# Performance work log

Measured on AMD Instinct MI355X. Metric: run time of the kernel, lower is better.

## Reference

```python
import jax, jax.numpy as jnp
import numpy as np

# YOLOv4 finest head: layer_no = 2 -> stride 8, anchor mask [0,1,2]
ANCHORS = np.array([[12,16],[19,36],[40,28],[36,75],[76,55],[72,146],[142,110],[192,243],[459,401]], dtype=np.float32)
STRIDE = 8.0
ANCH_MASK = (0, 1, 2)
N_CLASSES = 80
IGNORE_THRESH = 0.7


def setup_inputs() -> dict:
    key = jax.random.key(0)
    k1, k2, k3, k4, k5, k6, k7 = jax.random.split(key, 7)
    B, A, F = 32, 3, 76
    n_ch = 5 + N_CLASSES
    N = 50  # max padded boxes per image
    # 'output' feeds BCELoss -> must be probabilities in (0,1)
    output = jnp.clip(jax.random.uniform(k1, (B, A, F, F, n_ch)), 1e-4, 1.0 - 1e-4)
    # decoded pred boxes in grid units: xy in [0,F), wh > 0
    pxy = jax.random.uniform(k2, (B, A, F, F, 2)) * F
    pwh = jax.random.uniform(k3, (B, A, F, F, 2)) * 7.5 + 0.5
    pred = jnp.concatenate([pxy, pwh], axis=-1)
    # padded labels [cls, x, y, w, h] in pixels; first n rows valid, rest zero
    cls = jax.random.randint(k4, (B, N, 1), 0, N_CLASSES).astype(jnp.float32)
    xy = jax.random.uniform(k5, (B, N, 2)) * 604.0 + 2.0
    wh = jax.random.uniform(k6, (B, N, 2)) * 112.0 + 8.0
    labels = jnp.concatenate([cls, xy, wh], axis=-1)
    nvalid = jax.random.randint(k7, (B, 1), 5, N + 1)
    labels = labels * (jnp.arange(N)[None, :] < nvalid)[..., None].astype(jnp.float32)
    return {"output": output, "pred": pred, "labels": labels}


def _safe_log(x):
    # torch BCELoss clamps log terms at -100
    return jnp.maximum(jnp.log(jnp.maximum(x, 1e-43)), -100.0)


def _bce_sum(p, t, w):
    return -jnp.sum(w * (t * _safe_log(p) + (1.0 - t) * _safe_log(1.0 - p)))


def _yolo_layer_loss(output, pred, labels):
    B, A, F = output.shape[0], output.shape[1], output.shape[2]
    n_ch = output.shape[-1]
    N = labels.shape[1]
    dt = output.dtype
    ag = jnp.asarray(ANCHORS, dtype=dt) / STRIDE            # [9,2] anchors in grid units
    ma = ag[jnp.asarray(ANCH_MASK)]                          # [3,2] masked anchors

    valid = (labels.sum(-1) > 0)                             # [B,N] real (non-pad) boxes
    vf = valid.astype(dt)
    tx = labels[..., 1] / STRIDE
    ty = labels[..., 2] / STRIDE
    tw = labels[..., 3] / STRIDE
    th = labels[..., 4] / STRIDE
    ti = tx.astype(jnp.int32)
    tj = ty.astype(jnp.int32)
    twm, thm = tw * vf, th * vf                              # zero-area boxes for padding

    # --- anchor matching: IoU of [0,0,w,h] truth vs [0,0,w,h] reference anchors ---
    iw = jnp.minimum(twm[..., None], ag[:, 0])               # [B,N,9]
    ih = jnp.minimum(thm[..., None], ag[:, 1])
    en = ((iw > 0) & (ih > 0)).astype(dt)
    inter = iw * ih * en
    iou_a = inter / ((twm * thm)[..., None] + ag[:, 0] * ag[:, 1] - inter)
    best_all = jnp.argmax(iou_a, axis=-1)                    # [B,N]
    best_n = best_all % 3
    bmask = jnp.any(best_all[..., None] == jnp.asarray(ANCH_MASK), axis=-1)

    # --- ignore mask: IoU of all pred boxes vs truth boxes (xywh) ---
    pb = pred.reshape(B, -1, 4)                              # [B,M,4], M = A*F*F
    tbx, tby = tx * vf, ty * vf
    lx = jnp.maximum(pb[:, :, None, 0] - pb[:, :, None, 2] / 2, (tbx - twm / 2)[:, None, :])
    rx = jnp.minimum(pb[:, :, None, 0] + pb[:, :, None, 2] / 2, (tbx + twm / 2)[:, None, :])
    ly = jnp.maximum(pb[:, :, None, 1] - pb[:, :, None, 3] / 2, (tby - thm / 2)[:, None, :])
    ry = jnp.minimum(pb[:, :, None, 1] + pb[:, :, None, 3] / 2, (tby + thm / 2)[:, None, :])
    en_p = ((lx < rx) & (ly < ry)).astype(dt)
    inter_p = (rx - lx) * (ry - ly) * en_p                   # [B,M,N]
    area_p = pb[:, :, 2] * pb[:, :, 3]
    area_t = twm * thm
    iou_p = inter_p / (area_p[:, :, None] + area_t[:, None, :] - inter_p)
    best_iou = jnp.max(iou_p, axis=-1)                       # [B,M]
    obj0 = (1.0 - (best_iou > IGNORE_THRESH).astype(dt)).reshape(B, A, F, F)

    # --- scatter targets (pad trick: redirect unmatched writes to row/col F) ---
    write = bmask & valid
    bb = jnp.broadcast_to(jnp.arange(B)[:, None], (B, N)).reshape(-1)
    aa = best_n.reshape(-1)
    jj = jnp.where(write, tj, F).reshape(-1)
    ii = jnp.where(write, ti, F).reshape(-1)

    fx = tx - ti.astype(dt)
    fy = ty - tj.astype(dt)
    lw = jnp.log(tw / ma[best_n, 0] + 1e-16)
    lh = jnp.log(th / ma[best_n, 1] + 1e-16)
    oh = jax.nn.one_hot(labels[..., 0].astype(jnp.int32), N_CLASSES, dtype=dt)
    vec = jnp.concatenate([fx[..., None], fy[..., None], lw[..., None], lh[..., None],
                           jnp.ones_like(fx)[..., None], oh], axis=-1).reshape(B * N, n_ch)
    sc = jnp.sqrt(2.0 - tw * th / (F * F)).reshape(-1)

    tgt = jnp.zeros((B, A, F + 1, F + 1, n_ch), dt).at[bb, aa, jj, ii].set(vec)[:, :, :F, :F, :]
    msk = jnp.zeros((B, A, F + 1, F + 1), dt).at[bb, aa, jj, ii].set(1.0)[:, :, :F, :F]
    scl = jnp.zeros((B, A, F + 1, F + 1), dt).at[bb, aa, jj, ii].set(sc)[:, :, :F, :F]
    objm = jnp.pad(obj0, ((0, 0), (0, 0), (0, 1), (0, 1))).at[bb, aa, jj, ii].set(1.0)[:, :, :F, :F]

    m = msk[..., None]
    s = scl[..., None]
    # loss_xy: BCE with weight tgt_scale^2
    loss_xy = _bce_sum(output[..., :2] * m, tgt[..., :2] * m, s * s)
    # loss_wh: MSE/2 on scale-weighted wh
    dwh = output[..., 2:4] * m * s - tgt[..., 2:4] * m * s
    loss_wh = 0.5 * jnp.sum(dwh * dwh)
    # loss_obj / loss_cls: plain sum BCE
    loss_obj = _bce_sum(output[..., 4] * objm, tgt[..., 4] * objm, 1.0)
    loss_cls = _bce_sum(output[..., 5:] * m, tgt[..., 5:] * m, 1.0)
    return loss_xy + loss_wh + loss_obj + loss_cls


def reference(output, pred, labels):
    return _yolo_layer_loss(output, pred, labels)
```

## Files before the change

kernel.cpp:

```cpp
#include <hip/hip_runtime.h>
#include <cstdint>
#include <cstddef>

#define BB   32
#define AA   3
#define FF   76
#define NCH  85
#define NL   50
#define NCLS 80
#define CELLS (AA*FF*FF)
#define CPB  256
#define CPT  2
#define CELLS_PB (CPB*CPT)
#define BPB  ((CELLS + CELLS_PB - 1)/CELLS_PB)
#define GRID (BB*BPB)
#define NWAVE (CPB/64)


__global__ void __launch_bounds__(CPB) k_main(const float* __restrict__ outp,
                                              const float* __restrict__ pred,
                                              const float* __restrict__ labels,
                                              float* __restrict__ partial) {
    __shared__ float4 Sbox[NWAVE][NL];
    __shared__ float2 Sak[NWAVE][NL];
    __shared__ float  Srec[NWAVE][NL][6];
    __shared__ float  red[NWAVE];

    const float C717 = 0.7f / 1.7f;

    int bid  = blockIdx.x;
    int b    = bid / BPB;
    int blk  = bid % BPB;
    int base = blk * CELLS_PB;
    int wv   = threadIdx.x >> 6;
    int lane = threadIdx.x & 63;

    int    cell0 = base + (int)threadIdx.x;
    int    cell1 = cell0 + CPB;
    bool   live0 = cell0 < CELLS;
    bool   live1 = cell1 < CELLS;
    size_t ci0   = (size_t)b * CELLS + (size_t)(live0 ? cell0 : 0);
    size_t ci1   = (size_t)b * CELLS + (size_t)(live1 ? cell1 : 0);
    float4 pb0   = ((const float4*)pred)[ci0];
    float4 pb1   = ((const float4*)pred)[ci1];
    float  p40   = __builtin_nontemporal_load(outp + ci0 * NCH + 4);
    float  p41   = __builtin_nontemporal_load(outp + ci1 * NCH + 4);

    bool valid = false;
    {
        int  n   = lane;
        bool has = n < NL;
        if (has) {
            const float* L = labels + ((size_t)b * NL + n) * 5;
            float c0 = L[0], x = L[1], y = L[2], w = L[3], h = L[4];
            valid = (c0 + x + y + w + h) > 0.0f;
            float vf = valid ? 1.0f : 0.0f;

            float tx = x * 0.125f, ty = y * 0.125f;
            float tw = w * 0.125f, th = h * 0.125f;
            int   ti = (int)tx, tj = (int)ty;
            float twm = tw * vf, thm = th * vf;

            const float ag[9][2] = {
                {1.5f, 2.0f}, {2.375f, 4.5f}, {5.0f, 3.5f},
                {4.5f, 9.375f}, {9.5f, 6.875f}, {9.0f, 18.25f},
                {17.75f, 13.75f}, {24.0f, 30.375f}, {57.375f, 50.125f}
            };
            float at = twm * thm;
            float best = -1.0f; int bi = 0;
            #pragma unroll
            for (int k = 0; k < 9; ++k) {
                float iw = fminf(twm, ag[k][0]);
                float ih = fminf(thm, ag[k][1]);
                float inter = (iw > 0.0f && ih > 0.0f) ? iw * ih : 0.0f;
                float iou = inter * __builtin_amdgcn_rcpf(at + ag[k][0] * ag[k][1] - inter);
                if (iou > best) { best = iou; bi = k; }
            }
            int  bn    = bi % 3;
            bool write = (bi < 3) && valid;
            int  key   = write ? (bn * FF * FF + tj * FF + ti) : -1;

            float tbx = tx * vf, tby = ty * vf;
            Sbox[wv][n] = make_float4(tbx - twm * 0.5f, tbx + twm * 0.5f,
                                      tby - thm * 0.5f, tby + thm * 0.5f);
            Sak[wv][n]  = make_float2(twm * thm * C717, __int_as_float(key));
            Srec[wv][n][0] = tx - (float)ti;
            Srec[wv][n][1] = ty - (float)tj;
            Srec[wv][n][2] = __logf(tw * __builtin_amdgcn_rcpf(ag[bn][0]) + 1e-16f);
            Srec[wv][n][3] = __logf(th * __builtin_amdgcn_rcpf(ag[bn][1]) + 1e-16f);
            Srec[wv][n][4] = __builtin_amdgcn_sqrtf(2.0f - tw * th * (1.0f / (float)(FF * FF)));
            Srec[wv][n][5] = __int_as_float((int)L[0]);
        }
    }
    unsigned long long mb = __ballot(lane < NL && valid);
    int mx = mb ? (64 - __builtin_clzll(mb)) : 0;

    float plx0 = pb0.x - pb0.z * 0.5f, prx0 = pb0.x + pb0.z * 0.5f;
    float ply0 = pb0.y - pb0.w * 0.5f, pry0 = pb0.y + pb0.w * 0.5f;
    float apz0 = pb0.z * pb0.w * C717;
    float plx1 = pb1.x - pb1.z * 0.5f, prx1 = pb1.x + pb1.z * 0.5f;
    float ply1 = pb1.y - pb1.w * 0.5f, pry1 = pb1.y + pb1.w * 0.5f;
    float apz1 = pb1.z * pb1.w * C717;

    float md0 = -1e30f, md1 = -1e30f;
    int   mn0 = -1, mn1 = -1;
    for (int n = 0; n < mx; ++n) {
        float4 tb  = Sbox[wv][n];
        float2 ak  = Sak[wv][n];
        int    key = __float_as_int(ak.y);

        float lx0 = fmaxf(plx0, tb.x), rx0 = fminf(prx0, tb.y);
        float ly0 = fmaxf(ply0, tb.z), ry0 = fminf(pry0, tb.w);
        float w0 = fmaxf(rx0 - lx0, 0.0f), h0 = fmaxf(ry0 - ly0, 0.0f);
        md0 = fmaxf(md0, w0 * h0 - ak.x);
        if (key == cell0) mn0 = n;

        float lx1 = fmaxf(plx1, tb.x), rx1 = fminf(prx1, tb.y);
        float ly1 = fmaxf(ply1, tb.z), ry1 = fminf(pry1, tb.w);
        float w1 = fmaxf(rx1 - lx1, 0.0f), h1 = fmaxf(ry1 - ly1, 0.0f);
        md1 = fmaxf(md1, w1 * h1 - ak.x);
        if (key == cell1) mn1 = n;
    }

    float loss = 0.0f;
    #pragma unroll
    for (int c = 0; c < CPT; ++c) {
        bool   live = c ? live1 : live0;
        int    mn   = c ? mn1   : mn0;
        float  p4   = c ? p41   : p40;
        float  md   = c ? md1   : md0;
        float  apz  = c ? apz1  : apz0;
        size_t ci   = c ? ci1   : ci0;
        if (!live) continue;
        if (mn >= 0) {
            const float* op = outp + ci * NCH;
            const float* r  = Srec[wv][mn];
            loss += -__logf(p4);
            float s = r[4], s2 = s * s;
            float t0 = r[0], t1 = r[1];
            float p0 = op[0], p1 = op[1];
            loss += -s2 * (t0 * __logf(p0) + (1.0f - t0) * __logf(1.0f - p0));
            loss += -s2 * (t1 * __logf(p1) + (1.0f - t1) * __logf(1.0f - p1));
            float d0 = (op[2] - r[2]) * s;
            float d1 = (op[3] - r[3]) * s;
            loss += 0.5f * (d0 * d0 + d1 * d1);
            int   cls = __float_as_int(r[5]);
            float cl  = 0.0f;
            #pragma unroll
            for (int g = 0; g < NCLS / 8; ++g) {
                float pr = 1.0f;
                #pragma unroll
                for (int j = 0; j < 8; ++j) pr *= (1.0f - op[5 + g * 8 + j]);
                cl += __logf(pr);
            }
            float pc = op[5 + cls];
            loss += -cl + __logf(1.0f - pc) - __logf(pc);
        } else if (!(md > apz)) {
            loss += -__logf(1.0f - p4);
        }
    }

    #pragma unroll
    for (int off = 32; off > 0; off >>= 1) loss += __shfl_down(loss, off);
    if (lane == 0) red[wv] = loss;
    __syncthreads();
    if (threadIdx.x == 0)
        partial[bid] = red[0] + red[1] + red[2] + red[3];
}

__global__ void k_reduce(const float* __restrict__ partial, float* __restrict__ out) {
    __shared__ float red[256];
    float s = 0.0f;
    for (int i = threadIdx.x; i < GRID; i += 256) s += partial[i];
    red[threadIdx.x] = s;
    __syncthreads();
    for (int k = 128; k > 0; k >>= 1) {
        if ((int)threadIdx.x < k) red[threadIdx.x] += red[threadIdx.x + k];
        __syncthreads();
    }
    if (threadIdx.x == 0) out[0] = red[0];
}

extern "C" void kernel_launch(void* const* d_in, const int* in_sizes, int n_in,
                              void* d_out, int out_size, void* d_ws, size_t ws_size,
                              hipStream_t stream) {
    const float* outp   = (const float*)d_in[0];
    const float* pred   = (const float*)d_in[1];
    const float* labels = (const float*)d_in[2];

    float* partial = (float*)d_ws;

    k_main<<<GRID, CPB, 0, stream>>>(outp, pred, labels, partial);
    k_reduce<<<1, 256, 0, stream>>>(partial, (float*)d_out);
}
```

Measured before the change: 23.93 us.

## Fold final reduction into main kernel using per-block completion flags

Removes the separate single-block reduction kernel. Each block publishes its partial sum and then a release-stored DONE flag, and the last block spins on all flags before summing the partials. This is meant to save a kernel launch and the gap between the two kernels. The flags are never reset between calls, so from the second call on the last block can read stale partials from a previous run; it also relies on the last block not starving blocks that have not yet been scheduled.

```diff
diff --git a/kernel.cpp b/kernel.cpp
--- a/kernel.cpp
+++ b/kernel.cpp
@@ -15,16 +15,19 @@
 #define BPB  ((CELLS + CELLS_PB - 1)/CELLS_PB)
 #define GRID (BB*BPB)
 #define NWAVE (CPB/64)
+#define DONE 0x5A5A5A5Au
 
 
 __global__ void __launch_bounds__(CPB) k_main(const float* __restrict__ outp,
                                               const float* __restrict__ pred,
                                               const float* __restrict__ labels,
-                                              float* __restrict__ partial) {
+                                              float* __restrict__ partial,
+                                              unsigned* __restrict__ flag,
+                                              float* __restrict__ out) {
     __shared__ float4 Sbox[NWAVE][NL];
     __shared__ float2 Sak[NWAVE][NL];
     __shared__ float  Srec[NWAVE][NL][6];
-    __shared__ float  red[NWAVE];
+    __shared__ float  red[CPB / 64];
 
     const float C717 = 0.7f / 1.7f;
 
@@ -164,21 +167,32 @@
     for (int off = 32; off > 0; off >>= 1) loss += __shfl_down(loss, off);
     if (lane == 0) red[wv] = loss;
     __syncthreads();
-    if (threadIdx.x == 0)
-        partial[bid] = red[0] + red[1] + red[2] + red[3];
-}
-
-__global__ void k_reduce(const float* __restrict__ partial, float* __restrict__ out) {
-    __shared__ float red[256];
-    float s = 0.0f;
-    for (int i = threadIdx.x; i < GRID; i += 256) s += partial[i];
-    red[threadIdx.x] = s;
-    __syncthreads();
-    for (int k = 128; k > 0; k >>= 1) {
-        if ((int)threadIdx.x < k) red[threadIdx.x] += red[threadIdx.x + k];
+    if (threadIdx.x == 0) {
+        float bsum = red[0] + red[1] + red[2] + red[3];
+        __hip_atomic_store(&partial[bid], bsum, __ATOMIC_RELAXED, __HIP_MEMORY_SCOPE_AGENT);
+        __hip_atomic_store(&flag[bid], DONE, __ATOMIC_RELEASE, __HIP_MEMORY_SCOPE_AGENT);
+    }
+
+    if (bid == GRID - 1) {
+        for (int i = threadIdx.x; i < GRID; i += CPB) {
+            while (__hip_atomic_load(&flag[i], __ATOMIC_RELAXED, __HIP_MEMORY_SCOPE_AGENT) != DONE)
+                __builtin_amdgcn_s_sleep(2);
+        }
+        __threadfence();
         __syncthreads();
-    }
-    if (threadIdx.x == 0) out[0] = red[0];
+
+        __shared__ float fred[CPB];
+        float s = 0.0f;
+        for (int i = threadIdx.x; i < GRID; i += CPB)
+            s += __hip_atomic_load(&partial[i], __ATOMIC_RELAXED, __HIP_MEMORY_SCOPE_AGENT);
+        fred[threadIdx.x] = s;
+        __syncthreads();
+        for (int k = 128; k > 0; k >>= 1) {
+            if ((int)threadIdx.x < k) fred[threadIdx.x] += fred[threadIdx.x + k];
+            __syncthreads();
+        }
+        if (threadIdx.x == 0) out[0] = fred[0];
+    }
 }
 
 extern "C" void kernel_launch(void* const* d_in, const int* in_sizes, int n_in,
@@ -188,8 +202,8 @@
     const float* pred   = (const float*)d_in[1];
     const float* labels = (const float*)d_in[2];
 
-    float* partial = (float*)d_ws;
-
-    k_main<<<GRID, CPB, 0, stream>>>(outp, pred, labels, partial);
-    k_reduce<<<1, 256, 0, stream>>>(partial, (float*)d_out);
+    float*    partial = (float*)d_ws;
+    unsigned* flag    = (unsigned*)(partial + GRID);
+
+    k_main<<<GRID, CPB, 0, stream>>>(outp, pred, labels, partial, flag, (float*)d_out);
 }
```

Result: slower. 51.41 us (+114.9%).
